# Kernel tuning notes

Measured on AMD Instinct MI355X. Metric: run time of the kernel, lower is better.

The kernel has to match this reference:

```python
import jax, jax.numpy as jnp
import numpy as np

IOU_THRESHOLD = 0.5

def cxcywh_to_xyxy(b):
    cx, cy, w, h = jnp.split(b, 4, axis=-1)
    return jnp.concatenate([cx - 0.5 * w, cy - 0.5 * h, cx + 0.5 * w, cy + 0.5 * h], axis=-1)

def batched_giou(p_xyxy, t_xyxy):
    # p_xyxy: [B, N, 4], t_xyxy: [B, T, 4] -> giou: [B, N, T]
    p = p_xyxy[:, :, None, :]  # [B, N, 1, 4]
    t = t_xyxy[:, None, :, :]  # [B, 1, T, 4]
    area_p = (p_xyxy[..., 2] - p_xyxy[..., 0]) * (p_xyxy[..., 3] - p_xyxy[..., 1])  # [B, N]
    area_t = (t_xyxy[..., 2] - t_xyxy[..., 0]) * (t_xyxy[..., 3] - t_xyxy[..., 1])  # [B, T]
    lt = jnp.maximum(p[..., :2], t[..., :2])
    rb = jnp.minimum(p[..., 2:], t[..., 2:])
    wh = jnp.clip(rb - lt, 0.0)
    inter = wh[..., 0] * wh[..., 1]  # [B, N, T]
    union = area_p[:, :, None] + area_t[:, None, :] - inter
    iou = inter / union
    # enclosing box
    lt_e = jnp.minimum(p[..., :2], t[..., :2])
    rb_e = jnp.maximum(p[..., 2:], t[..., 2:])
    wh_e = jnp.clip(rb_e - lt_e, 0.0)
    area_e = wh_e[..., 0] * wh_e[..., 1]
    return iou - (area_e - union) / area_e

def setup_inputs() -> dict:
    key = jax.random.key(0)
    k1, k2 = jax.random.split(key)
    B, N, T = 128, 900, 300
    pred_boxes = jax.random.uniform(k1, (B, N, 4), dtype=jnp.float32)
    target_boxes = jax.random.uniform(k2, (B, T, 4), dtype=jnp.float32)
    target_mask = jnp.ones((B, T), dtype=bool)
    return {"pred_boxes": pred_boxes, "target_boxes": target_boxes, "target_mask": target_mask}

def reference(pred_boxes, target_boxes, target_mask):
    # pred_boxes: [B, N, 4] cxcywh; target_boxes: [B, T, 4] cxcywh (padded)
    p_xyxy = cxcywh_to_xyxy(pred_boxes)
    t_xyxy = cxcywh_to_xyxy(target_boxes)
    giou = batched_giou(p_xyxy, t_xyxy)  # [B, N, T]
    max_iou = jnp.max(giou, axis=1)      # [B, T] best GIoU per target
    pred_idx = jnp.argmax(giou, axis=1)  # [B, T] matched query per target
    valid = target_mask & (max_iou >= IOU_THRESHOLD)  # [B, T] match kept
    return pred_idx, valid, max_iou
```

## Files before the change

kernel.cpp:

```cpp
#include <hip/hip_runtime.h>


#define BB 128
#define NN 900
#define TT 300
#define TCHUNKS 5
#define WPB 8
#define MARGIN 2e-5f

__device__ __forceinline__ float giou_exact(float4 pb, float4 tb) {
#pragma clang fp contract(off)
    float px0 = pb.x - 0.5f * pb.z, py0 = pb.y - 0.5f * pb.w;
    float px1 = pb.x + 0.5f * pb.z, py1 = pb.y + 0.5f * pb.w;
    float tx0 = tb.x - 0.5f * tb.z, ty0 = tb.y - 0.5f * tb.w;
    float tx1 = tb.x + 0.5f * tb.z, ty1 = tb.y + 0.5f * tb.w;
    float pa = (px1 - px0) * (py1 - py0);
    float ta = (tx1 - tx0) * (ty1 - ty0);
    float w  = fmaxf(fminf(px1, tx1) - fmaxf(px0, tx0), 0.f);
    float h  = fmaxf(fminf(py1, ty1) - fmaxf(py0, ty0), 0.f);
    float inter = w * h;
    float uni   = pa + ta - inter;
    float iou   = inter / uni;
    float ew = fmaxf(fmaxf(px1, tx1) - fminf(px0, tx0), 0.f);
    float eh = fmaxf(fmaxf(py1, ty1) - fminf(py0, ty0), 0.f);
    float ea = ew * eh;
    return iou - (ea - uni) / ea;
}

__device__ __forceinline__ void giou_step(
    const float4 q,
    const float tx0, const float ty0, const float tx1, const float ty1,
    const float tw, const float th, const float ta, const int k,
    float& best, float& second, int& bidxl)
{
    const float pw = q.z - q.x;
    const float ph = q.w - q.y;
    const float pa = pw * ph;

    const float m1x = fminf(q.z, tx1);
    const float M0x = fmaxf(q.x, tx0);
    const float wr  = m1x - M0x;
    const float w   = fmaxf(wr, 0.f);
    const float m1y = fminf(q.w, ty1);
    const float M0y = fmaxf(q.y, ty0);
    const float hr  = m1y - M0y;
    const float h   = fmaxf(hr, 0.f);
    const float inter = w * h;
    const float uni   = (pa + ta) - inter;
    const float ew = (pw + tw) - wr;
    const float eh = (ph + th) - hr;
    const float ea = ew * eh;
    const float num = fmaf(inter, ea, uni * (uni - ea));
    const float g   = num * __builtin_amdgcn_rcpf(uni * ea);

    second = __builtin_amdgcn_fmed3f(g, best, second);
    if (g > best) bidxl = k;
    best = fmaxf(best, g);
}

__global__ __launch_bounds__(512, 4) void matcher_kernel(
    const float4* __restrict__ pred,
    const float4* __restrict__ tgt,
    const unsigned char* __restrict__ mask,
    float* __restrict__ out)
{
    __shared__ float4 sq[NN];
    __shared__ float rbv[512], rsv[512];
    __shared__ int   riv[512];
    __shared__ int   sflag[64];
    __shared__ int   scount;

    const int tc  = blockIdx.x % TCHUNKS;
    const int b   = blockIdx.x / TCHUNKS;
    const int tid = threadIdx.x;
    const int tl  = tid & 63;
    const int ng  = tid >> 6;

    if (tid == 0) scount = 0;

    for (int i = tid; i < NN; i += 512) {
        const float4 pb = pred[b * NN + i];
        float4 q;
        q.x = pb.x - 0.5f * pb.z;
        q.y = pb.y - 0.5f * pb.w;
        q.z = pb.x + 0.5f * pb.z;
        q.w = pb.y + 0.5f * pb.w;
        sq[i] = q;
    }
    __syncthreads();

    const int  t      = tc * 64 + tl;
    const bool tvalid = (t < TT);
    const float4 tb = tgt[b * TT + (tvalid ? t : 0)];
    const float tx0 = tb.x - 0.5f * tb.z;
    const float ty0 = tb.y - 0.5f * tb.w;
    const float tx1 = tb.x + 0.5f * tb.z;
    const float ty1 = tb.y + 0.5f * tb.w;
    const float tw  = tx1 - tx0;
    const float th  = ty1 - ty0;
    const float ta  = tw * th;

    const int k0 = ng * 112 + min(ng, 4);
    float best = -INFINITY, second = -INFINITY;
    int   bidxl = 0;
    #pragma unroll 8
    for (int k = 0; k < 112; ++k) {
        const float4 q = sq[k0 + k];
        giou_step(q, tx0, ty0, tx1, ty1, tw, th, ta, k, best, second, bidxl);
    }
    if (ng < 4) {
        const float4 q = sq[k0 + 112];
        giou_step(q, tx0, ty0, tx1, ty1, tw, th, ta, 112, best, second, bidxl);
    }
    int bidx = k0 + bidxl;

    rbv[tid] = best; rsv[tid] = second; riv[tid] = bidx;
    __syncthreads();

    if (ng == 0) {
        for (int s = 1; s < WPB; ++s) {
            const float ob = rbv[s * 64 + tl];
            const float os = rsv[s * 64 + tl];
            const int   oi = riv[s * 64 + tl];
            second = fmaxf(fminf(best, ob), fmaxf(second, os));
            if (ob > best) { best = ob; bidx = oi; }
        }

        if (tvalid) {
            const int bt = b * TT + t;
            if (best - second > MARGIN) {
                const float4 pb = pred[b * NN + bidx];
                const float4 tbr = tgt[bt];
                const float g = giou_exact(pb, tbr);
                const bool valid = (mask[bt] != 0) && (g >= 0.5f);
                out[bt]               = (float)bidx;
                out[BB * TT + bt]     = valid ? 1.f : 0.f;
                out[2 * BB * TT + bt] = g;
            } else {
                const int pos = atomicAdd(&scount, 1);
                sflag[pos] = tl;
            }
        }
    }
    __syncthreads();

    const int cnt = scount;
    for (int f = ng; f < cnt; f += WPB) {
        const int fbt = b * TT + tc * 64 + sflag[f];
        const float4 tbr = tgt[fbt];

        float bestx = -INFINITY;
        int   bix   = NN;
        for (int n = tl; n < NN; n += 64) {
            const float4 pb = pred[b * NN + n];
            const float g = giou_exact(pb, tbr);
            if (g > bestx) { bestx = g; bix = n; }
        }
        for (int off = 32; off >= 1; off >>= 1) {
            const float ob = __shfl_xor(bestx, off);
            const int   oi = __shfl_xor(bix, off);
            if (ob > bestx || (ob == bestx && oi < bix)) { bestx = ob; bix = oi; }
        }
        if (tl == 0) {
            const bool valid = (mask[fbt] != 0) && (bestx >= 0.5f);
            out[fbt]               = (float)bix;
            out[BB * TT + fbt]     = valid ? 1.f : 0.f;
            out[2 * BB * TT + fbt] = bestx;
        }
    }
}

extern "C" void kernel_launch(void* const* d_in, const int* in_sizes, int n_in,
                              void* d_out, int out_size, void* d_ws, size_t ws_size,
                              hipStream_t stream) {
    const float* pred = (const float*)d_in[0];
    const float* tgt  = (const float*)d_in[1];
    const unsigned char* mask = (const unsigned char*)d_in[2];
    float* out = (float*)d_out;

    matcher_kernel<<<dim3(BB * TCHUNKS), dim3(512), 0, stream>>>(
        (const float4*)pred, (const float4*)tgt, mask, out);
}
```

Baseline: 97.56 us.

## Broadcast pred boxes via readlane instead of staging them in LDS

Removes the shared-memory staging of converted prediction boxes and the block barrier that followed it. Each wave now loads its slice of up to 113 predictions directly into registers, one or two per lane, precomputes corners, width, height and area per lane, and broadcasts them to the whole wave with readlane (scalar registers) inside the inner loop. This drops per-iteration LDS reads and the per-box width/height/area recomputation, but adds seven readlanes per step, and the second loop now has a wave-uniform variable trip count that may unroll less cleanly.

```diff
diff --git a/kernel.cpp b/kernel.cpp
--- a/kernel.cpp
+++ b/kernel.cpp
@@ -7,6 +7,10 @@
 #define TCHUNKS 5
 #define WPB 8
 #define MARGIN 2e-5f
+
+__device__ __forceinline__ float rl(float v, int k) {
+    return __int_as_float(__builtin_amdgcn_readlane(__float_as_int(v), k));
+}
 
 __device__ __forceinline__ float giou_exact(float4 pb, float4 tb) {
 #pragma clang fp contract(off)
@@ -27,34 +31,31 @@
     return iou - (ea - uni) / ea;
 }
 
-__device__ __forceinline__ void giou_step(
-    const float4 q,
+__device__ __forceinline__ void giou_rl_step(
+    const float sx0, const float sy0, const float sx1, const float sy1,
+    const float spw, const float sph, const float spa,
     const float tx0, const float ty0, const float tx1, const float ty1,
-    const float tw, const float th, const float ta, const int k,
+    const float tw, const float th, const float ta, const int kidx,
     float& best, float& second, int& bidxl)
 {
-    const float pw = q.z - q.x;
-    const float ph = q.w - q.y;
-    const float pa = pw * ph;
-
-    const float m1x = fminf(q.z, tx1);
-    const float M0x = fmaxf(q.x, tx0);
+    const float m1x = fminf(sx1, tx1);
+    const float M0x = fmaxf(sx0, tx0);
     const float wr  = m1x - M0x;
     const float w   = fmaxf(wr, 0.f);
-    const float m1y = fminf(q.w, ty1);
-    const float M0y = fmaxf(q.y, ty0);
+    const float m1y = fminf(sy1, ty1);
+    const float M0y = fmaxf(sy0, ty0);
     const float hr  = m1y - M0y;
     const float h   = fmaxf(hr, 0.f);
     const float inter = w * h;
-    const float uni   = (pa + ta) - inter;
-    const float ew = (pw + tw) - wr;
-    const float eh = (ph + th) - hr;
+    const float uni   = (spa + ta) - inter;
+    const float ew = (spw + tw) - wr;
+    const float eh = (sph + th) - hr;
     const float ea = ew * eh;
     const float num = fmaf(inter, ea, uni * (uni - ea));
     const float g   = num * __builtin_amdgcn_rcpf(uni * ea);
 
     second = __builtin_amdgcn_fmed3f(g, best, second);
-    if (g > best) bidxl = k;
+    if (g > best) bidxl = kidx;
     best = fmaxf(best, g);
 }
 
@@ -64,7 +65,6 @@
     const unsigned char* __restrict__ mask,
     float* __restrict__ out)
 {
-    __shared__ float4 sq[NN];
     __shared__ float rbv[512], rsv[512];
     __shared__ int   riv[512];
     __shared__ int   sflag[64];
@@ -77,17 +77,6 @@
     const int ng  = tid >> 6;
 
     if (tid == 0) scount = 0;
-
-    for (int i = tid; i < NN; i += 512) {
-        const float4 pb = pred[b * NN + i];
-        float4 q;
-        q.x = pb.x - 0.5f * pb.z;
-        q.y = pb.y - 0.5f * pb.w;
-        q.z = pb.x + 0.5f * pb.z;
-        q.w = pb.y + 0.5f * pb.w;
-        sq[i] = q;
-    }
-    __syncthreads();
 
     const int  t      = tc * 64 + tl;
     const bool tvalid = (t < TT);
@@ -100,19 +89,48 @@
     const float th  = ty1 - ty0;
     const float ta  = tw * th;
 
-    const int k0 = ng * 112 + min(ng, 4);
+    const int k0u = __builtin_amdgcn_readfirstlane(
+        ng * 112 + (ng < 4 ? ng : 4));
+    const int n2u = __builtin_amdgcn_readfirstlane(ng < 4 ? 49 : 48);
+
+    const float4 pA = pred[b * NN + k0u + tl];
+    const int idxB  = k0u + 64 + tl;
+    const float4 pB = pred[b * NN + (idxB < NN ? idxB : NN - 1)];
+
+    const float qax0 = pA.x - 0.5f * pA.z;
+    const float qay0 = pA.y - 0.5f * pA.w;
+    const float qax1 = pA.x + 0.5f * pA.z;
+    const float qay1 = pA.y + 0.5f * pA.w;
+    const float qapw = qax1 - qax0;
+    const float qaph = qay1 - qay0;
+    const float qapa = qapw * qaph;
+
     float best = -INFINITY, second = -INFINITY;
     int   bidxl = 0;
     #pragma unroll 8
-    for (int k = 0; k < 112; ++k) {
-        const float4 q = sq[k0 + k];
-        giou_step(q, tx0, ty0, tx1, ty1, tw, th, ta, k, best, second, bidxl);
-    }
-    if (ng < 4) {
-        const float4 q = sq[k0 + 112];
-        giou_step(q, tx0, ty0, tx1, ty1, tw, th, ta, 112, best, second, bidxl);
-    }
-    int bidx = k0 + bidxl;
+    for (int k = 0; k < 64; ++k) {
+        giou_rl_step(rl(qax0, k), rl(qay0, k), rl(qax1, k), rl(qay1, k),
+                     rl(qapw, k), rl(qaph, k), rl(qapa, k),
+                     tx0, ty0, tx1, ty1, tw, th, ta, k,
+                     best, second, bidxl);
+    }
+
+    const float qbx0 = pB.x - 0.5f * pB.z;
+    const float qby0 = pB.y - 0.5f * pB.w;
+    const float qbx1 = pB.x + 0.5f * pB.z;
+    const float qby1 = pB.y + 0.5f * pB.w;
+    const float qbpw = qbx1 - qbx0;
+    const float qbph = qby1 - qby0;
+    const float qbpa = qbpw * qbph;
+
+    #pragma unroll 8
+    for (int k = 0; k < n2u; ++k) {
+        giou_rl_step(rl(qbx0, k), rl(qby0, k), rl(qbx1, k), rl(qby1, k),
+                     rl(qbpw, k), rl(qbph, k), rl(qbpa, k),
+                     tx0, ty0, tx1, ty1, tw, th, ta, 64 + k,
+                     best, second, bidxl);
+    }
+    int bidx = k0u + bidxl;
 
     rbv[tid] = best; rsv[tid] = second; riv[tid] = bidx;
     __syncthreads();
```

New measurement: 111.0 us. 1.14x slower.
